# Optimization experiments

Hardware: AMD Instinct MI355X
Metric: run time of the kernel (lower is better)

## Reference

```python
import jax, jax.numpy as jnp
import numpy as np

B = 4_000_000
N_LAYERS = 3


def _rot(phi, theta, omega):
    """PennyLane Rot(phi, theta, omega) = RZ(omega) @ RY(theta) @ RZ(phi), 2x2 complex64."""
    c = jnp.cos(theta * 0.5)
    s = jnp.sin(theta * 0.5)
    ep = jnp.exp(-0.5j * (phi + omega))  # e^{-i(phi+omega)/2}
    em = jnp.exp(0.5j * (phi - omega))   # e^{+i(phi-omega)/2}
    row0 = jnp.stack([ep * c, -em * s])
    row1 = jnp.stack([jnp.conj(em) * s, jnp.conj(ep) * c])
    return jnp.stack([row0, row1])  # [2, 2]


def _circuit(x, q_weights):
    # x: [B, 2] angles; q_weights: [3, 2, 3]
    half = x * 0.5
    c = jnp.cos(half)
    s = jnp.sin(half)
    # AngleEmbedding (default rotation='X') on |00>: product state of RX columns.
    u0 = jnp.stack([c[:, 0], -1j * s[:, 0]], axis=-1)  # [B, 2] complex64
    u1 = jnp.stack([c[:, 1], -1j * s[:, 1]], axis=-1)  # [B, 2]
    st = u0[:, :, None] * u1[:, None, :]               # [B, 2, 2] amplitudes (q0, q1)
    for l in range(N_LAYERS):
        U0 = _rot(q_weights[l, 0, 0], q_weights[l, 0, 1], q_weights[l, 0, 2])
        U1 = _rot(q_weights[l, 1, 0], q_weights[l, 1, 1], q_weights[l, 1, 2])
        st = jnp.einsum('ij,bjk->bik', U0, st)  # Rot on wire 0
        st = jnp.einsum('ij,bkj->bki', U1, st)  # Rot on wire 1
        # StronglyEntanglingLayers, 2 wires, range r=1: CNOT(0,1) then CNOT(1,0)
        st = jnp.stack([st[:, 0, :], st[:, 1, ::-1]], axis=1)  # CNOT ctrl=0, tgt=1
        st = jnp.stack([st[:, :, 0], st[:, ::-1, 1]], axis=2)  # CNOT ctrl=1, tgt=0
    p = jnp.abs(st) ** 2  # [B, 2, 2] real
    # <Z0> = P(q0=0) - P(q0=1)
    return (p[:, 0, :].sum(-1) - p[:, 1, :].sum(-1)).astype(jnp.float32)


def setup_inputs() -> dict:
    key = jax.random.key(0)
    k1, k2 = jax.random.split(key)
    x = jax.random.normal(k1, (B, 2), dtype=jnp.float32)
    q_weights = 0.01 * jax.random.normal(k2, (3, 2, 3), dtype=jnp.float32)
    return {"x": x, "q_weights": q_weights}


def reference(x, q_weights):
    return _circuit(x, q_weights)
```

## Files before the change

### kernel.cpp

```cpp
#include <hip/hip_runtime.h>
#include <math.h>


struct c32 { float re, im; };
__device__ __forceinline__ c32 cmul(c32 a, c32 b) { return { a.re*b.re - a.im*b.im, a.re*b.im + a.im*b.re }; }
__device__ __forceinline__ c32 cconj(c32 a) { return { a.re, -a.im }; }

__device__ __forceinline__ void build_G(const float* __restrict__ w, float* __restrict__ Gs)
{
    c32 M[4][4];
    #pragma unroll
    for (int i = 0; i < 4; ++i)
        #pragma unroll
        for (int j = 0; j < 4; ++j)
            M[i][j] = { (i == j) ? 1.f : 0.f, 0.f };

    #pragma unroll
    for (int l = 0; l < 3; ++l) {
        c32 U[2][2][2];
        #pragma unroll
        for (int q = 0; q < 2; ++q) {
            float phi   = w[(l*2 + q)*3 + 0];
            float theta = w[(l*2 + q)*3 + 1];
            float omega = w[(l*2 + q)*3 + 2];
            float c = __cosf(theta * 0.5f);
            float s = __sinf(theta * 0.5f);
            float ap = -0.5f * (phi + omega);
            float am =  0.5f * (phi - omega);
            c32 ep = { __cosf(ap), __sinf(ap) };
            c32 em = { __cosf(am), __sinf(am) };
            U[q][0][0] = {  ep.re * c,  ep.im * c };
            U[q][0][1] = { -em.re * s, -em.im * s };
            U[q][1][0] = {  em.re * s, -em.im * s };
            U[q][1][1] = {  ep.re * c, -ep.im * c };
        }
        c32 A[4][4];
        #pragma unroll
        for (int j = 0; j < 2; ++j)
            #pragma unroll
            for (int k = 0; k < 2; ++k)
                #pragma unroll
                for (int jp = 0; jp < 2; ++jp)
                    #pragma unroll
                    for (int kp = 0; kp < 2; ++kp)
                        A[2*j + k][2*jp + kp] = cmul(U[0][j][jp], U[1][k][kp]);
        #pragma unroll
        for (int col = 0; col < 4; ++col) { c32 t = A[2][col]; A[2][col] = A[3][col]; A[3][col] = t; }
        #pragma unroll
        for (int col = 0; col < 4; ++col) { c32 t = A[1][col]; A[1][col] = A[3][col]; A[3][col] = t; }
        c32 NM[4][4];
        #pragma unroll
        for (int i = 0; i < 4; ++i)
            #pragma unroll
            for (int j = 0; j < 4; ++j) {
                c32 acc = {0.f, 0.f};
                #pragma unroll
                for (int k = 0; k < 4; ++k) { c32 t = cmul(A[i][k], M[k][j]); acc.re += t.re; acc.im += t.im; }
                NM[i][j] = acc;
            }
        #pragma unroll
        for (int i = 0; i < 4; ++i)
            #pragma unroll
            for (int j = 0; j < 4; ++j) M[i][j] = NM[i][j];
    }

    const float Dv[4] = {1.f, 1.f, -1.f, -1.f};
    c32 H[4][4];
    #pragma unroll
    for (int a = 0; a < 4; ++a)
        #pragma unroll
        for (int b = 0; b < 4; ++b) {
            c32 acc = {0.f, 0.f};
            #pragma unroll
            for (int c = 0; c < 4; ++c) {
                c32 t = cmul(cconj(M[c][a]), M[c][b]);
                acc.re += Dv[c] * t.re;
                acc.im += Dv[c] * t.im;
            }
            H[a][b] = acc;
        }

    const c32 ph[4] = { {1.f,0.f}, {0.f,-1.f}, {0.f,-1.f}, {-1.f,0.f} };
    float K[16];
    #pragma unroll
    for (int a = 0; a < 4; ++a)
        #pragma unroll
        for (int b = 0; b < 4; ++b) {
            c32 f = cmul(cconj(ph[a]), ph[b]);
            K[a*4 + b] = f.re * H[a][b].re - f.im * H[a][b].im;
        }

    const float P[2][2][3] = { { {0.5f, 0.5f, 0.f}, {0.f, 0.f, 0.5f} },
                               { {0.f,  0.f, 0.5f}, {0.5f,-0.5f, 0.f} } };
    #pragma unroll
    for (int p = 0; p < 3; ++p)
        #pragma unroll
        for (int q = 0; q < 3; ++q) {
            float g = 0.f;
            #pragma unroll
            for (int i = 0; i < 2; ++i)
                #pragma unroll
                for (int k = 0; k < 2; ++k)
                    #pragma unroll
                    for (int j = 0; j < 2; ++j)
                        #pragma unroll
                        for (int l = 0; l < 2; ++l)
                            g += K[(2*i + j)*4 + (2*k + l)] * P[i][k][p] * P[j][l][q];
            Gs[p*3 + q] = g;
        }
}

__global__ __launch_bounds__(64, 1) void build_G_kernel(const float* __restrict__ w,
                                                        float* __restrict__ G)
{
    if (threadIdx.x == 0) build_G(w, G);
}

__device__ __forceinline__ float eval_pair(float x0, float x1,
                                           float G0, float G1, float G2,
                                           float G3, float G4, float G5,
                                           float G6, float G7, float G8)
{
    float C0 = __cosf(x0), S0 = __sinf(x0);
    float C1 = __cosf(x1), S1 = __sinf(x1);
    float t0 = G0 + G1*C1 + G2*S1;
    float t1 = G3 + G4*C1 + G5*S1;
    float t2 = G6 + G7*C1 + G8*S1;
    return t0 + C0*t1 + S0*t2;
}

__global__ __launch_bounds__(256, 4) void qmain(const float4* __restrict__ x4,
                                                const float* __restrict__ Gp,
                                                float2* __restrict__ out2,
                                                int nc2 , int B)
{
    const float G0 = Gp[0], G1 = Gp[1], G2 = Gp[2];
    const float G3 = Gp[3], G4 = Gp[4], G5 = Gp[5];
    const float G6 = Gp[6], G7 = Gp[7], G8 = Gp[8];

    const int S = (int)(gridDim.x * blockDim.x);
    const long long big = 4LL * S;
    for (long long base = (long long)blockIdx.x * blockDim.x + threadIdx.x;
         base < nc2; base += big) {
        const long long i0 = base;
        const long long i1 = base + S;
        const long long i2 = base + 2LL*S;
        const long long i3 = base + 3LL*S;
        if (i3 < nc2) {
            float4 v0 = x4[i0], v1 = x4[i1], v2 = x4[i2], v3 = x4[i3];
            out2[i0] = make_float2(eval_pair(v0.x, v0.y, G0,G1,G2,G3,G4,G5,G6,G7,G8),
                                   eval_pair(v0.z, v0.w, G0,G1,G2,G3,G4,G5,G6,G7,G8));
            out2[i1] = make_float2(eval_pair(v1.x, v1.y, G0,G1,G2,G3,G4,G5,G6,G7,G8),
                                   eval_pair(v1.z, v1.w, G0,G1,G2,G3,G4,G5,G6,G7,G8));
            out2[i2] = make_float2(eval_pair(v2.x, v2.y, G0,G1,G2,G3,G4,G5,G6,G7,G8),
                                   eval_pair(v2.z, v2.w, G0,G1,G2,G3,G4,G5,G6,G7,G8));
            out2[i3] = make_float2(eval_pair(v3.x, v3.y, G0,G1,G2,G3,G4,G5,G6,G7,G8),
                                   eval_pair(v3.z, v3.w, G0,G1,G2,G3,G4,G5,G6,G7,G8));
        } else {
            #pragma unroll
            for (int k = 0; k < 4; ++k) {
                long long i = base + (long long)k * S;
                if (i < nc2) {
                    float4 v = x4[i];
                    out2[i] = make_float2(eval_pair(v.x, v.y, G0,G1,G2,G3,G4,G5,G6,G7,G8),
                                          eval_pair(v.z, v.w, G0,G1,G2,G3,G4,G5,G6,G7,G8));
                }
            }
        }
    }

    if ((B & 1) && blockIdx.x == 0 && threadIdx.x == 0) {
        const float* x = (const float*)x4;
        float* out = (float*)out2;
        long long b = B - 1;
        out[b] = eval_pair(x[2*b], x[2*b+1], G0,G1,G2,G3,G4,G5,G6,G7,G8);
    }
}

extern "C" void kernel_launch(void* const* d_in, const int* in_sizes, int n_in,
                              void* d_out, int out_size, void* d_ws, size_t ws_size,
                              hipStream_t stream)
{
    const float* x = (const float*)d_in[0];
    const float* w = (const float*)d_in[1];
    float* out = (float*)d_out;
    float* G   = (float*)d_ws;
    const int B = in_sizes[0] / 2;
    const int nc2 = B >> 1;

    build_G_kernel<<<1, 64, 0, stream>>>(w, G);

    qmain<<<2048, 256, 0, stream>>>((const float4*)x, G, (float2*)out, nc2, B);
}
```

Baseline: 83.37 us.

## Fuse weight-matrix precompute into main kernel, parallelized across threads per block

Removes the separate single-thread build_G kernel launch and computes the 3x3 coefficient matrix redundantly inside every block. The work is split so 4 threads propagate unitary columns, 16 threads build the observable matrix, and 9 threads project to G, with shared memory and syncthreads between stages. This removes a launch and the serial dependency on a global workspace, at the cost of a short per-block prologue with three barriers. The grid size also drops from 2048 to 1024 blocks.

```diff
diff --git a/kernel.cpp b/kernel.cpp
--- a/kernel.cpp
+++ b/kernel.cpp
@@ -4,117 +4,7 @@
 
 struct c32 { float re, im; };
 __device__ __forceinline__ c32 cmul(c32 a, c32 b) { return { a.re*b.re - a.im*b.im, a.re*b.im + a.im*b.re }; }
-__device__ __forceinline__ c32 cconj(c32 a) { return { a.re, -a.im }; }
-
-__device__ __forceinline__ void build_G(const float* __restrict__ w, float* __restrict__ Gs)
-{
-    c32 M[4][4];
-    #pragma unroll
-    for (int i = 0; i < 4; ++i)
-        #pragma unroll
-        for (int j = 0; j < 4; ++j)
-            M[i][j] = { (i == j) ? 1.f : 0.f, 0.f };
-
-    #pragma unroll
-    for (int l = 0; l < 3; ++l) {
-        c32 U[2][2][2];
-        #pragma unroll
-        for (int q = 0; q < 2; ++q) {
-            float phi   = w[(l*2 + q)*3 + 0];
-            float theta = w[(l*2 + q)*3 + 1];
-            float omega = w[(l*2 + q)*3 + 2];
-            float c = __cosf(theta * 0.5f);
-            float s = __sinf(theta * 0.5f);
-            float ap = -0.5f * (phi + omega);
-            float am =  0.5f * (phi - omega);
-            c32 ep = { __cosf(ap), __sinf(ap) };
-            c32 em = { __cosf(am), __sinf(am) };
-            U[q][0][0] = {  ep.re * c,  ep.im * c };
-            U[q][0][1] = { -em.re * s, -em.im * s };
-            U[q][1][0] = {  em.re * s, -em.im * s };
-            U[q][1][1] = {  ep.re * c, -ep.im * c };
-        }
-        c32 A[4][4];
-        #pragma unroll
-        for (int j = 0; j < 2; ++j)
-            #pragma unroll
-            for (int k = 0; k < 2; ++k)
-                #pragma unroll
-                for (int jp = 0; jp < 2; ++jp)
-                    #pragma unroll
-                    for (int kp = 0; kp < 2; ++kp)
-                        A[2*j + k][2*jp + kp] = cmul(U[0][j][jp], U[1][k][kp]);
-        #pragma unroll
-        for (int col = 0; col < 4; ++col) { c32 t = A[2][col]; A[2][col] = A[3][col]; A[3][col] = t; }
-        #pragma unroll
-        for (int col = 0; col < 4; ++col) { c32 t = A[1][col]; A[1][col] = A[3][col]; A[3][col] = t; }
-        c32 NM[4][4];
-        #pragma unroll
-        for (int i = 0; i < 4; ++i)
-            #pragma unroll
-            for (int j = 0; j < 4; ++j) {
-                c32 acc = {0.f, 0.f};
-                #pragma unroll
-                for (int k = 0; k < 4; ++k) { c32 t = cmul(A[i][k], M[k][j]); acc.re += t.re; acc.im += t.im; }
-                NM[i][j] = acc;
-            }
-        #pragma unroll
-        for (int i = 0; i < 4; ++i)
-            #pragma unroll
-            for (int j = 0; j < 4; ++j) M[i][j] = NM[i][j];
-    }
-
-    const float Dv[4] = {1.f, 1.f, -1.f, -1.f};
-    c32 H[4][4];
-    #pragma unroll
-    for (int a = 0; a < 4; ++a)
-        #pragma unroll
-        for (int b = 0; b < 4; ++b) {
-            c32 acc = {0.f, 0.f};
-            #pragma unroll
-            for (int c = 0; c < 4; ++c) {
-                c32 t = cmul(cconj(M[c][a]), M[c][b]);
-                acc.re += Dv[c] * t.re;
-                acc.im += Dv[c] * t.im;
-            }
-            H[a][b] = acc;
-        }
-
-    const c32 ph[4] = { {1.f,0.f}, {0.f,-1.f}, {0.f,-1.f}, {-1.f,0.f} };
-    float K[16];
-    #pragma unroll
-    for (int a = 0; a < 4; ++a)
-        #pragma unroll
-        for (int b = 0; b < 4; ++b) {
-            c32 f = cmul(cconj(ph[a]), ph[b]);
-            K[a*4 + b] = f.re * H[a][b].re - f.im * H[a][b].im;
-        }
-
-    const float P[2][2][3] = { { {0.5f, 0.5f, 0.f}, {0.f, 0.f, 0.5f} },
-                               { {0.f,  0.f, 0.5f}, {0.5f,-0.5f, 0.f} } };
-    #pragma unroll
-    for (int p = 0; p < 3; ++p)
-        #pragma unroll
-        for (int q = 0; q < 3; ++q) {
-            float g = 0.f;
-            #pragma unroll
-            for (int i = 0; i < 2; ++i)
-                #pragma unroll
-                for (int k = 0; k < 2; ++k)
-                    #pragma unroll
-                    for (int j = 0; j < 2; ++j)
-                        #pragma unroll
-                        for (int l = 0; l < 2; ++l)
-                            g += K[(2*i + j)*4 + (2*k + l)] * P[i][k][p] * P[j][l][q];
-            Gs[p*3 + q] = g;
-        }
-}
-
-__global__ __launch_bounds__(64, 1) void build_G_kernel(const float* __restrict__ w,
-                                                        float* __restrict__ G)
-{
-    if (threadIdx.x == 0) build_G(w, G);
-}
+__device__ __forceinline__ c32 cadd(c32 a, c32 b) { return { a.re + b.re, a.im + b.im }; }
 
 __device__ __forceinline__ float eval_pair(float x0, float x1,
                                            float G0, float G1, float G2,
@@ -129,14 +19,119 @@
     return t0 + C0*t1 + S0*t2;
 }
 
-__global__ __launch_bounds__(256, 4) void qmain(const float4* __restrict__ x4,
-                                                const float* __restrict__ Gp,
-                                                float2* __restrict__ out2,
-                                                int nc2 , int B)
+__global__ __launch_bounds__(256, 4) void qfused2(const float4* __restrict__ x4,
+                                                  const float* __restrict__ w,
+                                                  float2* __restrict__ out2,
+                                                  int nc2 , int B)
 {
-    const float G0 = Gp[0], G1 = Gp[1], G2 = Gp[2];
-    const float G3 = Gp[3], G4 = Gp[4], G5 = Gp[5];
-    const float G6 = Gp[6], G7 = Gp[7], G8 = Gp[8];
+    __shared__ float Mc[4][8];
+    __shared__ float Ks[16];
+    __shared__ float Gs[9];
+
+    const int tid = threadIdx.x;
+
+    if (tid < 4) {
+        const int a = tid;
+        c32 col[4];
+        #pragma unroll
+        for (int c = 0; c < 4; ++c) col[c] = { (c == a) ? 1.f : 0.f, 0.f };
+
+        #pragma unroll
+        for (int l = 0; l < 3; ++l) {
+            c32 U0[2][2], U1[2][2];
+            #pragma unroll
+            for (int q = 0; q < 2; ++q) {
+                float phi   = w[(l*2 + q)*3 + 0];
+                float theta = w[(l*2 + q)*3 + 1];
+                float omega = w[(l*2 + q)*3 + 2];
+                float ch = __cosf(theta * 0.5f);
+                float sh = __sinf(theta * 0.5f);
+                float ap = -0.5f * (phi + omega);
+                float am =  0.5f * (phi - omega);
+                c32 ep = { __cosf(ap), __sinf(ap) };
+                c32 em = { __cosf(am), __sinf(am) };
+                c32 u00 = {  ep.re * ch,  ep.im * ch };
+                c32 u01 = { -em.re * sh, -em.im * sh };
+                c32 u10 = {  em.re * sh, -em.im * sh };
+                c32 u11 = {  ep.re * ch, -ep.im * ch };
+                if (q == 0) { U0[0][0]=u00; U0[0][1]=u01; U0[1][0]=u10; U0[1][1]=u11; }
+                else        { U1[0][0]=u00; U1[0][1]=u01; U1[1][0]=u10; U1[1][1]=u11; }
+            }
+            c32 t[2][2];
+            #pragma unroll
+            for (int jp = 0; jp < 2; ++jp)
+                #pragma unroll
+                for (int k = 0; k < 2; ++k)
+                    t[jp][k] = cadd(cmul(U1[k][0], col[2*jp + 0]),
+                                    cmul(U1[k][1], col[2*jp + 1]));
+            c32 pre[4];
+            #pragma unroll
+            for (int j = 0; j < 2; ++j)
+                #pragma unroll
+                for (int k = 0; k < 2; ++k)
+                    pre[2*j + k] = cadd(cmul(U0[j][0], t[0][k]),
+                                        cmul(U0[j][1], t[1][k]));
+            { c32 s = pre[2]; pre[2] = pre[3]; pre[3] = s; }
+            { c32 s = pre[1]; pre[1] = pre[3]; pre[3] = s; }
+            #pragma unroll
+            for (int c = 0; c < 4; ++c) col[c] = pre[c];
+        }
+        #pragma unroll
+        for (int c = 0; c < 4; ++c) { Mc[a][2*c] = col[c].re; Mc[a][2*c+1] = col[c].im; }
+    }
+    __syncthreads();
+
+    if (tid < 16) {
+        const int a = tid >> 2, b = tid & 3;
+        float Hre = 0.f, Him = 0.f;
+        #pragma unroll
+        for (int c = 0; c < 4; ++c) {
+            float ar = Mc[a][2*c], ai = Mc[a][2*c+1];
+            float br = Mc[b][2*c], bi = Mc[b][2*c+1];
+            float re = ar*br + ai*bi;
+            float im = ar*bi - ai*br;
+            float d = (c < 2) ? 1.f : -1.f;
+            Hre += d * re;
+            Him += d * im;
+        }
+        float par = (a == 0) ? 1.f : ((a == 3) ? -1.f : 0.f);
+        float pai = (a == 1 || a == 2) ? -1.f : 0.f;
+        float pbr = (b == 0) ? 1.f : ((b == 3) ? -1.f : 0.f);
+        float pbi = (b == 1 || b == 2) ? -1.f : 0.f;
+        c32 f = cmul({par, -pai}, {pbr, pbi});
+        Ks[tid] = f.re * Hre - f.im * Him;
+    }
+    __syncthreads();
+
+    if (tid < 9) {
+        const int p = (tid >= 6) ? 2 : ((tid >= 3) ? 1 : 0);
+        const int q = tid - 3*p;
+        float Pa[2][2], Pb[2][2];
+        Pa[0][0] = (p == 2) ? 0.f : 0.5f;
+        Pa[0][1] = (p == 2) ? 0.5f : 0.f;
+        Pa[1][0] = Pa[0][1];
+        Pa[1][1] = (p == 0) ? 0.5f : ((p == 1) ? -0.5f : 0.f);
+        Pb[0][0] = (q == 2) ? 0.f : 0.5f;
+        Pb[0][1] = (q == 2) ? 0.5f : 0.f;
+        Pb[1][0] = Pb[0][1];
+        Pb[1][1] = (q == 0) ? 0.5f : ((q == 1) ? -0.5f : 0.f);
+        float g = 0.f;
+        #pragma unroll
+        for (int i = 0; i < 2; ++i)
+            #pragma unroll
+            for (int k = 0; k < 2; ++k)
+                #pragma unroll
+                for (int j = 0; j < 2; ++j)
+                    #pragma unroll
+                    for (int l = 0; l < 2; ++l)
+                        g += Ks[(2*i + j)*4 + (2*k + l)] * Pa[i][k] * Pb[j][l];
+        Gs[tid] = g;
+    }
+    __syncthreads();
+
+    const float G0 = Gs[0], G1 = Gs[1], G2 = Gs[2];
+    const float G3 = Gs[3], G4 = Gs[4], G5 = Gs[5];
+    const float G6 = Gs[6], G7 = Gs[7], G8 = Gs[8];
 
     const int S = (int)(gridDim.x * blockDim.x);
     const long long big = 4LL * S;
@@ -184,11 +179,8 @@
     const float* x = (const float*)d_in[0];
     const float* w = (const float*)d_in[1];
     float* out = (float*)d_out;
-    float* G   = (float*)d_ws;
     const int B = in_sizes[0] / 2;
     const int nc2 = B >> 1;
 
-    build_G_kernel<<<1, 64, 0, stream>>>(w, G);
-
-    qmain<<<2048, 256, 0, stream>>>((const float4*)x, G, (float2*)out, nc2, B);
+    qfused2<<<1024, 256, 0, stream>>>((const float4*)x, w, (float2*)out, nc2, B);
 }
```

After: 79.17 us. -5.0%, faster.
